# Performance work log

Hardware: AMD Instinct MI355X
Metric: run time of the kernel (lower is better)

The kernel has to match this reference:

```python
import jax, jax.numpy as jnp
import numpy as np

B, N = 32, 1000
HID, COM = 256, 64
T_LEN, NOP = 288, 3
NVAL, TP_D, CS_D, TIME_D = 9, 2, 4, 4
IN_C = CS_D + TP_D + NVAL            # 15, competition GAT input
IN_CO = IN_C + COM                    # 79, cooperation GAT input
OBS = TIME_D + TP_D + CS_D + 2 * COM + NVAL  # 147
K_D = K_F = 500                       # int(0.5*N + 0.5)
TEMP = 1.0
NEG = jnp.float32(-1e8)


def setup_inputs() -> dict:
    key = jax.random.key(0)
    ks = jax.random.split(key, 24)
    def nrm(k, shp, scale=0.05):
        return (jax.random.normal(k, shp, dtype=jnp.float32) * scale)
    return {
        "time_idx": jax.random.randint(ks[0], (B, N), 0, T_LEN, dtype=jnp.int32),
        "op_idx": jax.random.randint(ks[1], (B, N), 0, NOP, dtype=jnp.int32),
        "value_feats": jax.random.normal(ks[2], (B, N, NVAL), dtype=jnp.float32),
        "dpcs_mark": jax.random.randint(ks[3], (B, N, 1), 0, 2) > 0,
        "adj_comp": jax.random.randint(ks[4], (B, N, N), 0, 2) > 0,
        "adj_coop": jax.random.randint(ks[5], (B, N, N), 0, 2) > 0,
        "distance": jax.random.uniform(ks[6], (N, N), dtype=jnp.float32),
        "time_tab": jax.random.uniform(ks[7], (T_LEN, TIME_D), dtype=jnp.float32),
        "tp_tab": jax.random.uniform(ks[8], (NOP, TP_D), dtype=jnp.float32),
        "cs_tab": jax.random.uniform(ks[9], (N, CS_D), dtype=jnp.float32),
        "Wc": nrm(ks[10], (IN_C, COM)),
        "asrc_c": nrm(ks[11], (COM,)),
        "adst_c": nrm(ks[12], (COM,)),
        "wd_c": jnp.float32(0.1),
        "Wco": nrm(ks[13], (IN_CO, COM)),
        "asrc_co": nrm(ks[14], (COM,)),
        "adst_co": nrm(ks[15], (COM,)),
        "wd_co": jnp.float32(0.1),
        "Wp": nrm(ks[16], (OBS, HID)),
        "bp": jnp.zeros((HID,), dtype=jnp.float32),
        "vpd": nrm(ks[17], (HID,)),
        "vpf": nrm(ks[18], (HID,)),
    }


def gat(x, W, a_src, a_dst, w_d, adj, dist):
    """Single-head GAT over dense boolean adjacency. adj[b,j,i] True => edge j->i."""
    h = jnp.einsum("bnf,fd->bnd", x, W)                       # (B,N,D)
    e = (jnp.einsum("bid,d->bi", h, a_dst)[:, :, None]        # dst term
         + jnp.einsum("bjd,d->bj", h, a_src)[:, None, :]      # src term
         + w_d * dist.T[None])                                 # dist[j,i] edge feat
    e = jax.nn.leaky_relu(e, 0.2)
    mask = jnp.swapaxes(adj, 1, 2)                             # (B, dst i, src j)
    e = jnp.where(mask, e, NEG)
    alpha = jax.nn.softmax(e, axis=-1)
    alpha = jnp.where(mask, alpha, 0.0)                        # isolated nodes -> 0
    return jax.nn.elu(jnp.einsum("bij,bjd->bid", alpha, h))


def gated_pool(x_p, scores, valid, k, temp):
    scores = scores - scores.max(axis=1, keepdims=True)
    scores = jnp.where(valid, scores, NEG)                     # (B,N,1)
    val_topk = jax.lax.top_k(scores[..., 0], k)[0]             # (B,k)
    min_topk = val_topk.min(axis=-1)[:, None, None]
    scores = jnp.where(scores < min_topk, NEG, scores)
    w = jax.nn.softmax(scores / temp, axis=1)
    xg = x_p * w
    return jnp.concatenate([xg.sum(axis=1), xg.max(axis=1)], axis=-1)  # (B,2H)


def reference(time_idx, op_idx, value_feats, dpcs_mark, adj_comp, adj_coop,
              distance, time_tab, tp_tab, cs_tab, Wc, asrc_c, adst_c, wd_c,
              Wco, asrc_co, adst_co, wd_co, Wp, bp, vpd, vpf):
    time_e = time_tab[time_idx]                                # (B,N,4)
    tp_e = tp_tab[op_idx]                                      # (B,N,2)
    cs_e = jnp.broadcast_to(cs_tab[None], (B, N, CS_D))        # (B,N,4)
    vf_det = jax.lax.stop_gradient(value_feats)
    x = jnp.concatenate([cs_e, tp_e, vf_det], axis=-1)         # (B,N,15)
    comp_reps = gat(x, Wc, asrc_c, adst_c, wd_c, adj_comp, distance)
    x_m = jnp.concatenate([x, comp_reps], axis=-1)             # (B,N,79)
    coop_reps = gat(x_m, Wco, asrc_co, adst_co, wd_co, adj_coop, distance)
    sag = jnp.concatenate([time_e, cs_e, tp_e, value_feats, comp_reps, coop_reps], axis=-1)
    x_p = jnp.einsum("bnf,fh->bnh", sag, Wp) + bp              # (B,N,HID)
    scores_d = jnp.einsum("bnh,h->bn", x_p, vpd)[..., None]
    s_d = gated_pool(x_p, scores_d, dpcs_mark, K_D, TEMP)
    scores_f = jnp.einsum("bnh,h->bn", x_p, vpf)[..., None]
    s_f = gated_pool(x_p, scores_f, ~dpcs_mark, K_F, TEMP)
    return jnp.concatenate([s_f, s_d], axis=-1)                # (B, 4*HID)
```

## Files before the change

kernel.cpp:

```cpp
#include <hip/hip_runtime.h>
#include <hip/hip_bf16.h>

#define NB 32
#define NN 1000
#define COMD 64
#define HIDD 256
#define KSEL 500
#define TI 16
#define NSPL 32
#define ROWS 32
#define DSTRIDE 1024

#define PB_DT   0
#define PB_AQ1  256
#define PB_AQ2  1280
#define PB_WP   2304
#define PB_WCO  2344
#define PB_MISC 2368
#define PB_N    2369

typedef __hip_bfloat16 bf16;
typedef unsigned long long u64;
typedef __attribute__((ext_vector_type(4))) float f32x4;
typedef __attribute__((ext_vector_type(8))) short s16x8;
typedef __attribute__((ext_vector_type(4))) short s16x4;
typedef __attribute__((ext_vector_type(4))) unsigned short u16x4;
typedef __attribute__((ext_vector_type(2))) unsigned long long u64x2;

__device__ __forceinline__ float b2f(bf16 x){ return __bfloat162float(x); }

template<bool F32>
__device__ __forceinline__ float ldf(const void* p, long i){
  return F32 ? ((const float*)p)[i] : b2f(((const bf16*)p)[i]);
}
template<bool BINT>
__device__ __forceinline__ bool ldb(const void* p, long i){
  return BINT ? (((const int*)p)[i] != 0) : (((const unsigned char*)p)[i] != 0);
}

__device__ __forceinline__ float wave_sum(float v){
#pragma unroll
  for (int o = 32; o > 0; o >>= 1) v += __shfl_down(v, o, 64);
  return v;
}
__device__ __forceinline__ float wave_bsum(float v){
#pragma unroll
  for (int o = 32; o > 0; o >>= 1) v += __shfl_xor(v, o, 64);
  return v;
}
__device__ __forceinline__ float wave_bmax(float v){
#pragma unroll
  for (int o = 32; o > 0; o >>= 1) v = fmaxf(v, __shfl_xor(v, o, 64));
  return v;
}
__device__ __forceinline__ int wave_bsum_i(int v){
#pragma unroll
  for (int o = 32; o > 0; o >>= 1) v += __shfl_xor(v, o, 64);
  return v;
}
__device__ __forceinline__ unsigned fkey(float f){
  unsigned u = __float_as_uint(f);
  return (u & 0x80000000u) ? ~u : (u | 0x80000000u);
}
__device__ __forceinline__ void split_bf(float v, short& hi, short& lo){
  unsigned u = __float_as_uint(v);
  float hf = __uint_as_float(u & 0xFFFF0000u);
  hi = (short)(u >> 16);
  float r = v - hf;
  lo = (short)(__float_as_uint(r) >> 16);
}
__device__ __forceinline__ short f2bs(float v){
  bf16 h = __float2bfloat16(v);
  short s; __builtin_memcpy(&s, &h, 2); return s;
}
__device__ __forceinline__ void hB_write(short* hB_hi, short* hB_lo,
                                         int b, int n, int ch, float v){
  int kb = n >> 5, g4 = (n >> 3) & 3, u = n & 7;
  long off = ((((long)b * 32 + kb) * 4 + g4) * 64 + ch) * 8 + u;
  short hi, lo; split_bf(v, hi, lo);
  hB_hi[off] = hi; hB_lo[off] = lo;
}
__device__ __forceinline__ void sniff2(const void* dist, const void* adjc,
                                       int lane, int& f32, int& as_int){
  unsigned wdist = ((const unsigned*)dist)[lane];
  unsigned wadj  = ((const unsigned*)adjc)[lane];
  f32 = (__ballot((wdist & 0xFFFFu) >= 0x8000u) != 0ull) ? 1 : 0;
  as_int = (__ballot(wadj > 1u) == 0ull) ? 1 : 0;
}

template<bool F32>
__device__ void dist_t_role(const void* dist, bf16* distTb, int rel){
  __shared__ bf16 tile[64][68];
  int t = threadIdx.x;
  int wv = t >> 6, lane = t & 63;
  int it = (rel & 15) * 64, jt = (rel >> 4) * 64;
#pragma unroll
  for (int r = 0; r < 16; ++r){
    int jl = r * 4 + wv;
    int j = jt + jl, i = it + lane;
    float v = (j < NN && i < NN) ? ldf<F32>(dist, (long)j * NN + i) : 0.f;
    tile[jl][lane] = __float2bfloat16(v);
  }
  __syncthreads();
#pragma unroll
  for (int r = 0; r < 16; ++r){
    int il = r * 4 + wv;
    int i = it + il, j = jt + lane;
    if (i < NN) distTb[(long)i * DSTRIDE + j] = tile[lane][il];
  }
}
template<bool BINT>
__device__ void adjq_role(const void* adj, u64* adjQ, int rel){
  __shared__ u64 aw[16][33];
  int t = threadIdx.x;
  int wv = t >> 6, lane = t & 63;
  int j0 = (rel & 31) * 32;
  int b  = rel >> 5;
  for (int r = 0; r < 8; ++r){
    int j = j0 + wv * 8 + r;
    int jc = (j < NN) ? j : (NN - 1);
    long row = ((long)b * NN + jc) * NN;
#pragma unroll
    for (int c = 0; c < 4; ++c){
      int chunk = c * 64 + lane;
      bool okc = chunk < 250;
      bool p0, p1, p2, p3;
      if (BINT){
        uint4 d = {0u, 0u, 0u, 0u};
        if (okc) d = *(const uint4*)((const int*)adj + row + (long)chunk * 4);
        p0 = d.x != 0u; p1 = d.y != 0u; p2 = d.z != 0u; p3 = d.w != 0u;
      } else {
        unsigned d = 0u;
        if (okc) d = *(const unsigned*)((const unsigned char*)adj + row + (long)chunk * 4);
        p0 = (d & 0xFFu) != 0u;       p1 = (d & 0xFF00u) != 0u;
        p2 = (d & 0xFF0000u) != 0u;   p3 = (d & 0xFF000000u) != 0u;
      }
      u64 bal0 = __ballot(p0), bal1 = __ballot(p1);
      u64 bal2 = __ballot(p2), bal3 = __ballot(p3);
      if (lane < 4){
        u64 w = 0;
        if (j < NN){
          int sh = 16 * lane;
          w = ((bal0 >> sh) & 0xFFFFull)
            | (((bal1 >> sh) & 0xFFFFull) << 16)
            | (((bal2 >> sh) & 0xFFFFull) << 32)
            | (((bal3 >> sh) & 0xFFFFull) << 48);
        }
        aw[c * 4 + lane][wv * 8 + r] = w;
      }
    }
  }
  __syncthreads();
#pragma unroll
  for (int rr = 0; rr < 2; ++rr){
    int w2 = t + rr * 256;
    int iw = w2 >> 5, jloc = w2 & 31;
    adjQ[((long)b * 16 + iw) * 1024 + j0 + jloc] = aw[iw][jloc];
  }
}
template<bool F32>
__device__ void wp_role(const void* Wp, const void* vpd, const void* vpf,
                        short* WpB_hi, short* WpB_lo, float* wv_ws, int rel){
  int t = threadIdx.x;
  int g = t >> 6, lane = t & 63;
  int f = rel * 4 + g;
  float wrow[4];
#pragma unroll
  for (int r = 0; r < 4; ++r){
    int ch = r * 64 + lane;
    wrow[r] = (f < 147) ? ldf<F32>(Wp, (long)f * HIDD + ch) : 0.f;
  }
  int kb = f >> 5, q = (f >> 3) & 3, u = f & 7;
#pragma unroll
  for (int r = 0; r < 4; ++r){
    int ch = r * 64 + lane;
    long off = (((long)(kb * 4 + q)) * 256 + ch) * 8 + u;
    short hi, lo; split_bf(wrow[r], hi, lo);
    WpB_hi[off] = hi; WpB_lo[off] = lo;
  }
  float ad = 0.f, af = 0.f;
#pragma unroll
  for (int r = 0; r < 4; ++r){
    int ch = r * 64 + lane;
    ad += wrow[r] * ldf<F32>(vpd, ch);
    af += wrow[r] * ldf<F32>(vpf, ch);
  }
  ad = wave_bsum(ad); af = wave_bsum(af);
  if (lane == 0){ wv_ws[f] = ad; wv_ws[160 + f] = af; }
}
template<bool F32>
__device__ void wco_role(const void* Wco, const void* asrc, const void* adst,
                         short* WcoB_hi, short* WcoB_lo, float* pvco, int rel){
  int t = threadIdx.x;
  int g = t >> 6, lane = t & 63;
  int f = rel * 4 + g;
  float w = (f < 79) ? ldf<F32>(Wco, (long)f * COMD + lane) : 0.f;
  int kb = f >> 5, q = (f >> 3) & 3, u = f & 7;
  long off = (((long)(kb * 4 + q)) * 64 + lane) * 8 + u;
  short hi, lo; split_bf(w, hi, lo);
  WcoB_hi[off] = hi; WcoB_lo[off] = lo;
  float dd = wave_bsum(w * ldf<F32>(adst, lane));
  float ss = wave_bsum(w * ldf<F32>(asrc, lane));
  if (lane == 0){ pvco[f] = dd; pvco[96 + f] = ss; }
}
template<bool F32>
__device__ void misc_role(const void* wdc, const void* wdco,
                          const void* bp, const void* vpd, const void* vpf,
                          int f32, int as_int,
                          int* flags, float* wd_ws, float* wv_ws){
  int t = threadIdx.x;
  if (t >= 64) return;
  int lane = t;
  float ad = 0.f, af = 0.f;
#pragma unroll
  for (int r = 0; r < 4; ++r){
    int ch = r * 64 + lane;
    float bb = ldf<F32>(bp, ch);
    ad += bb * ldf<F32>(vpd, ch);
    af += bb * ldf<F32>(vpf, ch);
  }
  ad = wave_bsum(ad); af = wave_bsum(af);
  if (lane == 0){
    wv_ws[320] = ad; wv_ws[321] = af;
    wd_ws[0] = ldf<F32>(wdc, 0);
    wd_ws[1] = ldf<F32>(wdco, 0);
    flags[0] = f32; flags[1] = as_int;
  }
}
__global__ void __launch_bounds__(256) k_prep(
    const void* dist, const void* adj_comp, const void* adj_coop,
    const void* wdc, const void* wdco,
    const void* Wp, const void* vpd, const void* vpf, const void* bp,
    const void* Wco, const void* asrc_co, const void* adst_co,
    int* flags, float* wd_ws, bf16* distTb, u64* adjQc, u64* adjQo,
    short* WpB_hi, short* WpB_lo, float* wv_ws,
    short* WcoB_hi, short* WcoB_lo, float* pvco){
  int blk = blockIdx.x;
  int f32, as_int;
  sniff2(dist, adj_comp, threadIdx.x & 63, f32, as_int);
  if (blk < PB_AQ1){
    if (f32) dist_t_role<true >(dist, distTb, blk);
    else     dist_t_role<false>(dist, distTb, blk);
  } else if (blk < PB_AQ2){
    if (as_int) adjq_role<true >(adj_comp, adjQc, blk - PB_AQ1);
    else        adjq_role<false>(adj_comp, adjQc, blk - PB_AQ1);
  } else if (blk < PB_WP){
    if (as_int) adjq_role<true >(adj_coop, adjQo, blk - PB_AQ2);
    else        adjq_role<false>(adj_coop, adjQo, blk - PB_AQ2);
  } else if (blk < PB_WCO){
    if (f32) wp_role<true >(Wp, vpd, vpf, WpB_hi, WpB_lo, wv_ws, blk - PB_WP);
    else     wp_role<false>(Wp, vpd, vpf, WpB_hi, WpB_lo, wv_ws, blk - PB_WP);
  } else if (blk < PB_MISC){
    if (f32) wco_role<true >(Wco, asrc_co, adst_co, WcoB_hi, WcoB_lo, pvco, blk - PB_WCO);
    else     wco_role<false>(Wco, asrc_co, adst_co, WcoB_hi, WcoB_lo, pvco, blk - PB_WCO);
  } else {
    if (f32) misc_role<true >(wdc, wdco, bp, vpd, vpf, f32, as_int, flags, wd_ws, wv_ws);
    else     misc_role<false>(wdc, wdco, bp, vpd, vpf, f32, as_int, flags, wd_ws, wv_ws);
  }
}

template<bool F32>
__device__ __forceinline__ void embed_body(
    const int* op_idx, const void* vf, const void* cs_tab, const void* tp_tab,
    const void* Wc, const void* asrc, const void* adst,
    float* x_out, short* hB_hi, short* hB_lo, float* ed_out, float* es_out){
  int t = threadIdx.x;
  int w = t >> 6, lane = t & 63;
  int g = blockIdx.x * 4 + w;
  int b = g / NN, n = g - b * NN;
  int op = op_idx[g];
  float xv = 0.f, hacc = 0.f;
#pragma unroll
  for (int f = 0; f < 15; ++f){
    float x_f;
    if (f < 4)      x_f = ldf<F32>(cs_tab, n * 4 + f);
    else if (f < 6) x_f = ldf<F32>(tp_tab, op * 2 + (f - 4));
    else            x_f = ldf<F32>(vf, (long)g * 9 + (f - 6));
    if (lane == f) xv = x_f;
    hacc += x_f * ldf<F32>(Wc, f * COMD + lane);
  }
  if (lane < 15) x_out[g * 15 + lane] = xv;
  hB_write(hB_hi, hB_lo, b, n, lane, hacc);
  float sd = wave_sum(hacc * ldf<F32>(adst, lane));
  float ss = wave_sum(hacc * ldf<F32>(asrc, lane));
  if (lane == 0){ ed_out[g] = sd; es_out[g] = ss; }
}
__global__ void __launch_bounds__(256) k_embed(
    const int* flags, const int* op_idx, const void* vf, const void* cs_tab,
    const void* tp_tab, const void* Wc, const void* asrc, const void* adst,
    float* x_out, short* hB_hi, short* hB_lo, float* ed_out, float* es_out){
  if (flags[0]) embed_body<true >(op_idx, vf, cs_tab, tp_tab, Wc, asrc, adst, x_out, hB_hi, hB_lo, ed_out, es_out);
  else          embed_body<false>(op_idx, vf, cs_tab, tp_tab, Wc, asrc, adst, x_out, hB_hi, hB_lo, ed_out, es_out);
}

__global__ void __launch_bounds__(256) k_hco(
    const float* __restrict__ x_ws, const float* __restrict__ comp,
    const short* __restrict__ WcoB_hi, const short* __restrict__ WcoB_lo,
    const float* __restrict__ pvco,
    short* hB_hi, short* hB_lo, float* ed_out, float* es_out){
  __shared__ float cx[16][80] __attribute__((aligned(16)));
  __shared__ short cA_hi[3 * 16 * 40] __attribute__((aligned(16)));
  __shared__ short cA_lo[3 * 16 * 40] __attribute__((aligned(16)));
  int t = threadIdx.x;
  int wv = t >> 6, lane = t & 63;
  int base = blockIdx.x * 16;
  for (int idx = t; idx < 16 * 79; idx += 256){
    int nl = idx / 79, f = idx - nl * 79;
    int g = base + nl;
    cx[nl][f] = (f < 15) ? x_ws[g * 15 + f] : comp[(long)g * COMD + (f - 15)];
  }
  __syncthreads();
  {
    int node = t >> 4, sub = t & 15;
    float dd = 0.f, ss = 0.f;
    for (int f = sub; f < 79; f += 16){
      float c = cx[node][f];
      dd += c * pvco[f];
      ss += c * pvco[96 + f];
    }
#pragma unroll
    for (int o = 8; o > 0; o >>= 1){
      dd += __shfl_xor(dd, o, 64);
      ss += __shfl_xor(ss, o, 64);
    }
    if (sub == 0){
      int g = base + node;
      ed_out[g] = dd; es_out[g] = ss;
    }
  }
  for (int idx = t; idx < 16 * 96; idx += 256){
    int m = idx / 96, k = idx - m * 96;
    float v = (k < 79) ? cx[m][k] : 0.f;
    int kb = k >> 5, q = (k >> 3) & 3, u = k & 7;
    short hi, lo; split_bf(v, hi, lo);
    int off = (kb * 16 + m) * 40 + q * 8 + u;
    cA_hi[off] = hi; cA_lo[off] = lo;
  }
  __syncthreads();
  int q = lane >> 4, m = lane & 15;
  int ch = wv * 16 + m;
  f32x4 acc = {0.f, 0.f, 0.f, 0.f};
#pragma unroll
  for (int kb = 0; kb < 3; ++kb){
    int aoff = (kb * 16 + m) * 40 + q * 8;
    s16x8 a_hi = *(const s16x8*)&cA_hi[aoff];
    s16x8 a_lo = *(const s16x8*)&cA_lo[aoff];
    long boff = (((long)(kb * 4 + q)) * 64 + ch) * 8;
    s16x8 b_hi = *(const s16x8*)&WcoB_hi[boff];
    s16x8 b_lo = *(const s16x8*)&WcoB_lo[boff];
    acc = __builtin_amdgcn_mfma_f32_16x16x32_bf16(a_hi, b_hi, acc, 0, 0, 0);
    acc = __builtin_amdgcn_mfma_f32_16x16x32_bf16(a_hi, b_lo, acc, 0, 0, 0);
    acc = __builtin_amdgcn_mfma_f32_16x16x32_bf16(a_lo, b_hi, acc, 0, 0, 0);
  }
#pragma unroll
  for (int reg = 0; reg < 4; ++reg){
    int row = (lane >> 4) * 4 + reg;
    int g = base + row;
    int b = g / NN, n = g - b * NN;
    hB_write(hB_hi, hB_lo, b, n, ch, acc[reg]);
  }
}

__global__ void __launch_bounds__(256) k_gat(
    const float* __restrict__ ed, const float* __restrict__ es,
    const float* __restrict__ wd_ws, int wd_idx, const u64* __restrict__ adjQ,
    const bf16* __restrict__ distTb,
    const short* __restrict__ hB_hi, const short* __restrict__ hB_lo,
    float* __restrict__ reps){
  __shared__ short pA[32 * 544] __attribute__((aligned(16)));
  __shared__ float redz[TI][4];
  __shared__ float esred[4];
  int t = threadIdx.x;
  int wv = t >> 6, lane = t & 63;
  int b = blockIdx.y;
  int i0 = blockIdx.x * TI;
  float wd = wd_ws[wd_idx];
  int iw = i0 >> 6;
  int sb2 = (i0 & 63) >> 2;
  int j0 = t * 4;

  const u64* aq = adjQ + ((long)b * 16 + iw) * 1024 + j0;
  u64x2 wA = *(const u64x2*)&aq[0];
  u64x2 wB = *(const u64x2*)&aq[2];
  u64 wsh[4] = { wA[0] >> sb2, wA[1] >> sb2, wB[0] >> sb2, wB[1] >> sb2 };
  float4 es4 = *(const float4*)&es[(long)b * NN + j0];
  float esv[4] = {es4.x, es4.y, es4.z, es4.w};
  float esm = -1e30f;
#pragma unroll
  for (int c = 0; c < 4; ++c)
    esm = fmaxf(esm, (j0 + c < NN) ? esv[c] : -1e30f);
  esm = wave_bmax(esm);
  if (lane == 0) esred[wv] = esm;

  float ed_i[TI]; float edm = -1e30f;
#pragma unroll
  for (int ti = 0; ti < TI; ++ti){
    int i = i0 + ti;
    float ev = ed[(long)b * NN + ((i < NN) ? i : (NN - 1))];
    ed_i[ti] = ev;
    edm = fmaxf(edm, (i < NN) ? ev : -1e30f);
  }
  __syncthreads();
  float M = fmaxf(fmaxf(esred[0], esred[1]), fmaxf(esred[2], esred[3]))
            + edm + fmaxf(wd, 0.f);
  M = fmaxf(M, 0.f);

  float p[TI][4];
  const bf16* dbase = distTb + j0;
#pragma unroll
  for (int ti = 0; ti < TI; ++ti){
    int i = i0 + ti;
    int ic = (i < NN) ? i : (NN - 1);
    u16x4 d4 = *(const u16x4*)&dbase[(long)ic * DSTRIDE];
    float edti = ed_i[ti];
    int psh = 16 * (ti & 3) + (ti >> 2);
#pragma unroll
    for (int c = 0; c < 4; ++c){
      float d = __uint_as_float((unsigned)d4[c] << 16);
      float v = edti + esv[c] + wd * d;
      v = fmaxf(v, 0.2f * v);
      bool edge = (wsh[c] >> psh) & 1ull;
      float e = edge ? v : -1e30f;
      p[ti][c] = __expf(e - M);
    }
  }

  int kbw = 8 * wv + (lane >> 3);
  int qw = (lane >> 1) & 3;
  int u0 = 4 * (lane & 1);
  int wbase = kbw * 544 + qw * 136 + u0;
#pragma unroll
  for (int ti = 0; ti < TI; ++ti){
    float zs = p[ti][0] + p[ti][1] + p[ti][2] + p[ti][3];
    zs = wave_bsum(zs);
    if (lane == 0) redz[ti][wv] = zs;
    s16x4 s4 = { f2bs(p[ti][0]), f2bs(p[ti][1]), f2bs(p[ti][2]), f2bs(p[ti][3]) };
    *(s16x4*)&pA[wbase + ti * 8] = s4;
  }
  __syncthreads();

  int q = lane >> 4, m = lane & 15;
  int abase = q * 136 + m * 8;
  int ch = wv * 16 + m;
  const short* bh = hB_hi + (long)b * 65536 + ((long)q * 64 + ch) * 8;
  const short* bl = hB_lo + (long)b * 65536 + ((long)q * 64 + ch) * 8;
  f32x4 acc = {0.f, 0.f, 0.f, 0.f};
#pragma unroll
  for (int kb = 0; kb < 32; ++kb){
    s16x8 a   = *(const s16x8*)&pA[kb * 544 + abase];
    s16x8 bhi = *(const s16x8*)&bh[(long)kb * 2048];
    s16x8 blo = *(const s16x8*)&bl[(long)kb * 2048];
    acc = __builtin_amdgcn_mfma_f32_16x16x32_bf16(a, bhi, acc, 0, 0, 0);
    acc = __builtin_amdgcn_mfma_f32_16x16x32_bf16(a, blo, acc, 0, 0, 0);
  }
#pragma unroll
  for (int reg = 0; reg < 4; ++reg){
    int ti = (lane >> 4) * 4 + reg;
    float z = redz[ti][0] + redz[ti][1] + redz[ti][2] + redz[ti][3];
    float zi = (z > 0.f) ? 1.f / z : 0.f;
    float v = acc[reg] * zi;
    v = (v > 0.f) ? v : expm1f(v);
    int ch2 = wv * 16 + (lane & 15);
    if (i0 + ti < NN)
      reps[((long)b * NN + i0 + ti) * COMD + ch2] = v;
  }
}

template<bool F32>
__device__ __forceinline__ void xp_body(
    const int* time_idx, const int* op_idx, const void* vf, const void* time_tab,
    const void* cs_tab, const void* tp_tab, const float* comp, const float* coop,
    const short* __restrict__ WpB_hi, const short* __restrict__ WpB_lo,
    const float* __restrict__ wv_ws, const void* bp,
    float* x_p, float* scf, float* scd){
  __shared__ float sagF[16][148] __attribute__((aligned(16)));
  __shared__ short sagA_hi[5 * 16 * 40] __attribute__((aligned(16)));
  __shared__ short sagA_lo[5 * 16 * 40] __attribute__((aligned(16)));
  int t = threadIdx.x;
  int wv = t >> 6, lane = t & 63;
  int base = blockIdx.x * 16;

  for (int idx = t; idx < 16 * 147; idx += 256){
    int nl = idx / 147, f = idx - nl * 147;
    int g = base + nl;
    int n = g % NN;
    float v;
    if (f < 4)       v = ldf<F32>(time_tab, time_idx[g] * 4 + f);
    else if (f < 8)  v = ldf<F32>(cs_tab, n * 4 + (f - 4));
    else if (f < 10) v = ldf<F32>(tp_tab, op_idx[g] * 2 + (f - 8));
    else if (f < 19) v = ldf<F32>(vf, (long)g * 9 + (f - 10));
    else if (f < 83) v = comp[(long)g * COMD + (f - 19)];
    else             v = coop[(long)g * COMD + (f - 83)];
    sagF[nl][f] = v;
  }
  __syncthreads();

  for (int idx = t; idx < 16 * 160; idx += 256){
    int m = idx / 160, k = idx - m * 160;
    float v = (k < 147) ? sagF[m][k] : 0.f;
    int kb = k >> 5, q = (k >> 3) & 3, u = k & 7;
    short hi, lo; split_bf(v, hi, lo);
    int off = (kb * 16 + m) * 40 + q * 8 + u;
    sagA_hi[off] = hi; sagA_lo[off] = lo;
  }
  {
    int node = t >> 4, sub = t & 15;
    float ad = 0.f, af = 0.f;
    for (int f = sub; f < 147; f += 16){
      float s = sagF[node][f];
      ad += s * wv_ws[f];
      af += s * wv_ws[160 + f];
    }
#pragma unroll
    for (int o = 8; o > 0; o >>= 1){
      ad += __shfl_xor(ad, o, 64);
      af += __shfl_xor(af, o, 64);
    }
    if (sub == 0){
      scd[base + node] = ad + wv_ws[320];
      scf[base + node] = af + wv_ws[321];
    }
  }
  __syncthreads();

  int Ag = lane >> 4, Am = lane & 15;
  f32x4 acc[4] = {{0,0,0,0},{0,0,0,0},{0,0,0,0},{0,0,0,0}};
#pragma unroll
  for (int kb = 0; kb < 5; ++kb){
    int aoff = (kb * 16 + Am) * 40 + Ag * 8;
    s16x8 a_hi = *(const s16x8*)&sagA_hi[aoff];
    s16x8 a_lo = *(const s16x8*)&sagA_lo[aoff];
#pragma unroll
    for (int ct = 0; ct < 4; ++ct){
      int ch = wv * 64 + ct * 16 + Am;
      long boff = (((long)(kb * 4 + Ag)) * 256 + ch) * 8;
      s16x8 b_hi = *(const s16x8*)&WpB_hi[boff];
      s16x8 b_lo = *(const s16x8*)&WpB_lo[boff];
      acc[ct] = __builtin_amdgcn_mfma_f32_16x16x32_bf16(a_hi, b_hi, acc[ct], 0, 0, 0);
      acc[ct] = __builtin_amdgcn_mfma_f32_16x16x32_bf16(a_hi, b_lo, acc[ct], 0, 0, 0);
      acc[ct] = __builtin_amdgcn_mfma_f32_16x16x32_bf16(a_lo, b_hi, acc[ct], 0, 0, 0);
    }
  }
#pragma unroll
  for (int ct = 0; ct < 4; ++ct){
    int ch = wv * 64 + ct * 16 + (lane & 15);
    float bb = ldf<F32>(bp, ch);
#pragma unroll
    for (int reg = 0; reg < 4; ++reg){
      int row = (lane >> 4) * 4 + reg;
      x_p[(long)(base + row) * HIDD + ch] = acc[ct][reg] + bb;
    }
  }
}
__global__ void __launch_bounds__(256) k_xp(
    const int* flags, const int* time_idx, const int* op_idx, const void* vf,
    const void* time_tab, const void* cs_tab, const void* tp_tab,
    const float* comp, const float* coop,
    const short* WpB_hi, const short* WpB_lo, const float* wv_ws, const void* bp,
    float* x_p, float* scf, float* scd){
  if (flags[0]) xp_body<true >(time_idx, op_idx, vf, time_tab, cs_tab, tp_tab, comp, coop, WpB_hi, WpB_lo, wv_ws, bp, x_p, scf, scd);
  else          xp_body<false>(time_idx, op_idx, vf, time_tab, cs_tab, tp_tab, comp, coop, WpB_hi, WpB_lo, wv_ws, bp, x_p, scf, scd);
}

template<bool BINT>
__device__ __forceinline__ void topk_body(
    const float* scf, const float* scd, const void* mark, float* wls){
  int lane = threadIdx.x;
  int b = blockIdx.x, pool = blockIdx.y;
  const float* sc = (pool == 0) ? scf : scd;
  float v[16]; unsigned key[16];
  float m0 = -INFINITY;
#pragma unroll
  for (int r = 0; r < 16; ++r){
    int n = r * 64 + lane;
    float s = (n < NN) ? sc[b * NN + n] : -INFINITY;
    v[r] = s;
    m0 = fmaxf(m0, s);
  }
  m0 = wave_bmax(m0);
  float m1 = -INFINITY;
#pragma unroll
  for (int r = 0; r < 16; ++r){
    int n = r * 64 + lane;
    bool valid = false;
    if (n < NN){
      bool mk = ldb<BINT>(mark, b * NN + n);
      valid = (pool == 0) ? !mk : mk;
    }
    v[r] = valid ? (v[r] - m0) : -1e8f;
    key[r] = fkey(v[r]);
    if (n < NN) m1 = fmaxf(m1, v[r]);
  }
  m1 = wave_bmax(m1);

  unsigned lo = 0u, hi = 0xFFFFFFFFu;
  while (lo < hi){
    unsigned mid = lo + ((hi - lo) >> 1) + 1u;
    int c = 0;
#pragma unroll
    for (int r = 0; r < 16; ++r) c += (key[r] >= mid) ? 1 : 0;
    c = wave_bsum_i(c);
    if (c >= KSEL) lo = mid; else hi = mid - 1u;
  }

  float p[16];
  float ls = 0.f;
#pragma unroll
  for (int r = 0; r < 16; ++r){
    int n = r * 64 + lane;
    float pp = (n < NN && key[r] >= lo) ? __expf(v[r] - m1) : 0.f;
    p[r] = pp;
    ls += pp;
  }
  ls = wave_bsum(ls);
  float zinv = (ls > 0.f) ? 1.f / ls : 0.f;
  float* w_out = wls + ((long)b * 2 + pool) * 1024;
#pragma unroll
  for (int r = 0; r < 16; ++r){
    int n = r * 64 + lane;
    if (n < NN) w_out[n] = p[r] * zinv;
  }
}
__global__ void k_topk(const int* flags, const float* scf, const float* scd,
                       const void* mark, float* wls){
  if (flags[1]) topk_body<true >(scf, scd, mark, wls);
  else          topk_body<false>(scf, scd, mark, wls);
}

__global__ void __launch_bounds__(256) k_psum(
    const float* __restrict__ wls, const float* __restrict__ x_p,
    float* __restrict__ part){
  __shared__ float wf[ROWS], wdd[ROWS];
  int t = threadIdx.x;
  int b = blockIdx.x, z = blockIdx.y;
  int n0 = z * ROWS;
  int ns = min(ROWS, NN - n0);
  if (t < ns){
    wf[t]  = wls[((long)b * 2 + 0) * 1024 + n0 + t];
    wdd[t] = wls[((long)b * 2 + 1) * 1024 + n0 + t];
  }
  __syncthreads();
  float sf = 0.f, mf = -INFINITY, sd = 0.f, md = -INFINITY;
  const float* xb = x_p + ((long)b * NN + n0) * HIDD + t;
  for (int k = 0; k < ns; ++k){
    float xv = xb[(long)k * HIDD];
    float gf = wf[k] * xv;
    float gd = wdd[k] * xv;
    sf += gf; mf = fmaxf(mf, gf);
    sd += gd; md = fmaxf(md, gd);
  }
  long pb = (((long)b * NSPL + z) * 4) * HIDD + t;
  part[pb + 0 * HIDD] = sf;
  part[pb + 1 * HIDD] = mf;
  part[pb + 2 * HIDD] = sd;
  part[pb + 3 * HIDD] = md;
}

template<bool F32>
__device__ __forceinline__ void pfin_body(const float* part, void* out){
  int t = threadIdx.x;
  int b = blockIdx.x;
  float sf = 0.f, mf = -INFINITY, sd = 0.f, md = -INFINITY;
#pragma unroll
  for (int z = 0; z < NSPL; ++z){
    long pb = (((long)b * NSPL + z) * 4) * HIDD + t;
    sf += part[pb + 0 * HIDD];
    mf = fmaxf(mf, part[pb + 1 * HIDD]);
    sd += part[pb + 2 * HIDD];
    md = fmaxf(md, part[pb + 3 * HIDD]);
  }
  long ob = (long)b * 1024;
  if (F32){
    ((float*)out)[ob + t] = sf;
    ((float*)out)[ob + 256 + t] = mf;
    ((float*)out)[ob + 512 + t] = sd;
    ((float*)out)[ob + 768 + t] = md;
  } else {
    ((bf16*)out)[ob + t] = __float2bfloat16(sf);
    ((bf16*)out)[ob + 256 + t] = __float2bfloat16(mf);
    ((bf16*)out)[ob + 512 + t] = __float2bfloat16(sd);
    ((bf16*)out)[ob + 768 + t] = __float2bfloat16(md);
  }
}
__global__ void k_pfin(const int* flags, const float* part, void* out){
  if (flags[0]) pfin_body<true >(part, out);
  else          pfin_body<false>(part, out);
}

extern "C" void kernel_launch(void* const* d_in, const int* in_sizes, int n_in,
                              void* d_out, int out_size, void* d_ws, size_t ws_size,
                              hipStream_t stream){
  const int*  time_idx = (const int*)d_in[0];
  const int*  op_idx   = (const int*)d_in[1];
  const void* vfeat    = d_in[2];
  const void* dpcs     = d_in[3];
  const void* adj_comp = d_in[4];
  const void* adj_coop = d_in[5];
  const void* dist     = d_in[6];
  const void* time_tab = d_in[7];
  const void* tp_tab   = d_in[8];
  const void* cs_tab   = d_in[9];
  const void* Wc       = d_in[10];
  const void* asrc_c   = d_in[11];
  const void* adst_c   = d_in[12];
  const void* wd_c     = d_in[13];
  const void* Wco      = d_in[14];
  const void* asrc_co  = d_in[15];
  const void* adst_co  = d_in[16];
  const void* wd_co    = d_in[17];
  const void* Wp       = d_in[18];
  const void* bp       = d_in[19];
  const void* vpd      = d_in[20];
  const void* vpf      = d_in[21];

  char* ws = (char*)d_ws;
  size_t o = 0;
  auto alloc = [&](size_t bytes)->char*{
    char* p = ws + o; o = (o + bytes + 255) & ~(size_t)255; return p;
  };
  int*   flags   = (int*)alloc(16);
  float* wd_ws   = (float*)alloc(8);
  bf16*  distTb  = (bf16*)alloc((size_t)NN * DSTRIDE * 2);
  u64*   adjQc   = (u64*)alloc((size_t)NB * 16 * 1024 * 8);
  u64*   adjQo   = (u64*)alloc((size_t)NB * 16 * 1024 * 8);
  float* x_ws    = (float*)alloc((size_t)NB * NN * 15 * 4);
  float* comp    = (float*)alloc((size_t)NB * NN * COMD * 4);
  float* coop    = (float*)alloc((size_t)NB * NN * COMD * 4);
  short* hB_hi   = (short*)alloc((size_t)NB * 65536 * 2);
  short* hB_lo   = (short*)alloc((size_t)NB * 65536 * 2);
  short* WpB_hi  = (short*)alloc((size_t)5 * 4 * 256 * 8 * 2);
  short* WpB_lo  = (short*)alloc((size_t)5 * 4 * 256 * 8 * 2);
  short* WcoB_hi = (short*)alloc((size_t)3 * 4 * 64 * 8 * 2);
  short* WcoB_lo = (short*)alloc((size_t)3 * 4 * 64 * 8 * 2);
  float* wv_ws   = (float*)alloc(322 * 4);
  float* pvco    = (float*)alloc(192 * 4);
  float* ed_c    = (float*)alloc((size_t)NB * NN * 4 + 256);
  float* es_c    = (float*)alloc((size_t)NB * NN * 4 + 256);
  float* ed_o    = (float*)alloc((size_t)NB * NN * 4 + 256);
  float* es_o    = (float*)alloc((size_t)NB * NN * 4 + 256);
  float* scf     = (float*)alloc((size_t)NB * NN * 4);
  float* scd     = (float*)alloc((size_t)NB * NN * 4);
  float* wls     = (float*)alloc((size_t)NB * 2 * 1024 * 4);
  float* part    = (float*)alloc((size_t)NB * NSPL * 4 * HIDD * 4);
  float* x_p     = (float*)alloc((size_t)NB * NN * HIDD * 4);

  k_prep<<<dim3(PB_N), dim3(256), 0, stream>>>(
      dist, adj_comp, adj_coop, wd_c, wd_co, Wp, vpd, vpf, bp,
      Wco, asrc_co, adst_co,
      flags, wd_ws, distTb, adjQc, adjQo, WpB_hi, WpB_lo, wv_ws,
      WcoB_hi, WcoB_lo, pvco);
  k_embed<<<dim3(NB * NN / 4), dim3(256), 0, stream>>>(
      flags, op_idx, vfeat, cs_tab, tp_tab, Wc, asrc_c, adst_c,
      x_ws, hB_hi, hB_lo, ed_c, es_c);
  k_gat<<<dim3((NN + TI - 1) / TI, NB), dim3(256), 0, stream>>>(
      ed_c, es_c, wd_ws, 0, adjQc, distTb, hB_hi, hB_lo, comp);
  k_hco<<<dim3(NB * NN / 16), dim3(256), 0, stream>>>(
      x_ws, comp, WcoB_hi, WcoB_lo, pvco, hB_hi, hB_lo, ed_o, es_o);
  k_gat<<<dim3((NN + TI - 1) / TI, NB), dim3(256), 0, stream>>>(
      ed_o, es_o, wd_ws, 1, adjQo, distTb, hB_hi, hB_lo, coop);
  k_xp<<<dim3(NB * NN / 16), dim3(256), 0, stream>>>(
      flags, time_idx, op_idx, vfeat, time_tab, cs_tab, tp_tab, comp, coop,
      WpB_hi, WpB_lo, wv_ws, bp, x_p, scf, scd);
  k_topk<<<dim3(NB, 2), dim3(64), 0, stream>>>(flags, scf, scd, dpcs, wls);
  k_psum<<<dim3(NB, NSPL), dim3(256), 0, stream>>>(wls, x_p, part);
  k_pfin<<<dim3(NB), dim3(256), 0, stream>>>(flags, part, d_out);
}
```

Measured before the change: 494.9 us.

## Fuse embed kernel into prep kernel and prefetch adjacency rows

The embed work becomes extra blocks of the prep kernel, removing one launch and letting it overlap with the adjacency packing. The embed blocks now use the f32 sniff result computed locally instead of reading flags written by an earlier kernel. Adjacency packing now double-buffers row loads so the next row's loads are in flight while the current one is balloted. Block roles are reordered so adjacency blocks come first, and the shared-memory tiles are merged into one buffer. This adds register pressure and a much larger combined grid.

New measurement: 487.6 us. About the same (-1.5%).

```diff
diff --git a/kernel.cpp b/kernel.cpp
--- a/kernel.cpp
+++ b/kernel.cpp
@@ -11,13 +11,14 @@
 #define ROWS 32
 #define DSTRIDE 1024
 
-#define PB_DT   0
-#define PB_AQ1  256
-#define PB_AQ2  1280
+#define PB_AQ1  0
+#define PB_AQ2  1024
+#define PB_DT   2048
 #define PB_WP   2304
 #define PB_WCO  2344
 #define PB_MISC 2368
-#define PB_N    2369
+#define PB_EMB  2369
+#define PB_N    (PB_EMB + NB * NN / 4)
 
 typedef __hip_bfloat16 bf16;
 typedef unsigned long long u64;
@@ -88,9 +89,12 @@
   as_int = (__ballot(wadj > 1u) == 0ull) ? 1 : 0;
 }
 
+#define SMEM_BYTES 8704
+
 template<bool F32>
-__device__ void dist_t_role(const void* dist, bf16* distTb, int rel){
-  __shared__ bf16 tile[64][68];
+__device__ __forceinline__ void dist_t_role(const void* dist, bf16* distTb,
+                                            int rel, void* sm){
+  bf16 (*tile)[68] = (bf16 (*)[68])sm;
   int t = threadIdx.x;
   int wv = t >> 6, lane = t & 63;
   int it = (rel & 15) * 64, jt = (rel >> 4) * 64;
@@ -110,43 +114,99 @@
   }
 }
 template<bool BINT>
-__device__ void adjq_role(const void* adj, u64* adjQ, int rel){
-  __shared__ u64 aw[16][33];
+__device__ __forceinline__ void adjq_role(const void* adj, u64* adjQ,
+                                          int rel, void* sm){
+  u64 (*aw)[33] = (u64 (*)[33])sm;
   int t = threadIdx.x;
   int wv = t >> 6, lane = t & 63;
   int j0 = (rel & 31) * 32;
   int b  = rel >> 5;
-  for (int r = 0; r < 8; ++r){
-    int j = j0 + wv * 8 + r;
+  int ch3 = (192 + lane < 250) ? (192 + lane) : 249;
+  int chk[4] = { lane, 64 + lane, 128 + lane, ch3 };
+  long row0;
+  {
+    int j = j0 + wv * 8;
     int jc = (j < NN) ? j : (NN - 1);
-    long row = ((long)b * NN + jc) * NN;
-#pragma unroll
-    for (int c = 0; c < 4; ++c){
-      int chunk = c * 64 + lane;
-      bool okc = chunk < 250;
-      bool p0, p1, p2, p3;
-      if (BINT){
-        uint4 d = {0u, 0u, 0u, 0u};
-        if (okc) d = *(const uint4*)((const int*)adj + row + (long)chunk * 4);
-        p0 = d.x != 0u; p1 = d.y != 0u; p2 = d.z != 0u; p3 = d.w != 0u;
-      } else {
-        unsigned d = 0u;
-        if (okc) d = *(const unsigned*)((const unsigned char*)adj + row + (long)chunk * 4);
-        p0 = (d & 0xFFu) != 0u;       p1 = (d & 0xFF00u) != 0u;
-        p2 = (d & 0xFF0000u) != 0u;   p3 = (d & 0xFF000000u) != 0u;
+    row0 = ((long)b * NN + jc) * (long)NN;
+  }
+  if (BINT){
+    const int* base = (const int*)adj;
+    uint4 cur[4], nxt[4];
+#pragma unroll
+    for (int c = 0; c < 4; ++c)
+      cur[c] = *(const uint4*)(base + row0 + (long)chk[c] * 4);
+#pragma unroll
+    for (int r = 0; r < 8; ++r){
+      if (r < 7){
+        int j2 = j0 + wv * 8 + r + 1;
+        int jc2 = (j2 < NN) ? j2 : (NN - 1);
+        long row2 = ((long)b * NN + jc2) * (long)NN;
+#pragma unroll
+        for (int c = 0; c < 4; ++c)
+          nxt[c] = *(const uint4*)(base + row2 + (long)chk[c] * 4);
       }
-      u64 bal0 = __ballot(p0), bal1 = __ballot(p1);
-      u64 bal2 = __ballot(p2), bal3 = __ballot(p3);
-      if (lane < 4){
-        u64 w = 0;
-        if (j < NN){
-          int sh = 16 * lane;
-          w = ((bal0 >> sh) & 0xFFFFull)
-            | (((bal1 >> sh) & 0xFFFFull) << 16)
-            | (((bal2 >> sh) & 0xFFFFull) << 32)
-            | (((bal3 >> sh) & 0xFFFFull) << 48);
+      int j = j0 + wv * 8 + r;
+#pragma unroll
+      for (int c = 0; c < 4; ++c){
+        u64 bal0 = __ballot(cur[c].x != 0u);
+        u64 bal1 = __ballot(cur[c].y != 0u);
+        u64 bal2 = __ballot(cur[c].z != 0u);
+        u64 bal3 = __ballot(cur[c].w != 0u);
+        if (lane < 4){
+          u64 w = 0;
+          if (j < NN){
+            int sh = 16 * lane;
+            w = ((bal0 >> sh) & 0xFFFFull)
+              | (((bal1 >> sh) & 0xFFFFull) << 16)
+              | (((bal2 >> sh) & 0xFFFFull) << 32)
+              | (((bal3 >> sh) & 0xFFFFull) << 48);
+          }
+          aw[c * 4 + lane][wv * 8 + r] = w;
         }
-        aw[c * 4 + lane][wv * 8 + r] = w;
+      }
+      if (r < 7){
+#pragma unroll
+        for (int c = 0; c < 4; ++c) cur[c] = nxt[c];
+      }
+    }
+  } else {
+    const unsigned char* base = (const unsigned char*)adj;
+    unsigned cur[4], nxt[4];
+#pragma unroll
+    for (int c = 0; c < 4; ++c)
+      cur[c] = *(const unsigned*)(base + row0 + (long)chk[c] * 4);
+#pragma unroll
+    for (int r = 0; r < 8; ++r){
+      if (r < 7){
+        int j2 = j0 + wv * 8 + r + 1;
+        int jc2 = (j2 < NN) ? j2 : (NN - 1);
+        long row2 = ((long)b * NN + jc2) * (long)NN;
+#pragma unroll
+        for (int c = 0; c < 4; ++c)
+          nxt[c] = *(const unsigned*)(base + row2 + (long)chk[c] * 4);
+      }
+      int j = j0 + wv * 8 + r;
+#pragma unroll
+      for (int c = 0; c < 4; ++c){
+        u64 bal0 = __ballot((cur[c] & 0xFFu) != 0u);
+        u64 bal1 = __ballot((cur[c] & 0xFF00u) != 0u);
+        u64 bal2 = __ballot((cur[c] & 0xFF0000u) != 0u);
+        u64 bal3 = __ballot((cur[c] & 0xFF000000u) != 0u);
+        if (lane < 4){
+          u64 w = 0;
+          if (j < NN){
+            int sh = 16 * lane;
+            w = ((bal0 >> sh) & 0xFFFFull)
+              | (((bal1 >> sh) & 0xFFFFull) << 16)
+              | (((bal2 >> sh) & 0xFFFFull) << 32)
+              | (((bal3 >> sh) & 0xFFFFull) << 48);
+          }
+          aw[c * 4 + lane][wv * 8 + r] = w;
+        }
+      }
+      if (r < 7){
+#pragma unroll
+        for (int c = 0; c < 4; ++c) cur[c] = nxt[c];
       }
     }
   }
@@ -159,7 +219,7 @@
   }
 }
 template<bool F32>
-__device__ void wp_role(const void* Wp, const void* vpd, const void* vpf,
+__device__ __forceinline__ void wp_role(const void* Wp, const void* vpd, const void* vpf,
                         short* WpB_hi, short* WpB_lo, float* wv_ws, int rel){
   int t = threadIdx.x;
   int g = t >> 6, lane = t & 63;
@@ -189,7 +249,7 @@
   if (lane == 0){ wv_ws[f] = ad; wv_ws[160 + f] = af; }
 }
 template<bool F32>
-__device__ void wco_role(const void* Wco, const void* asrc, const void* adst,
+__device__ __forceinline__ void wco_role(const void* Wco, const void* asrc, const void* adst,
                          short* WcoB_hi, short* WcoB_lo, float* pvco, int rel){
   int t = threadIdx.x;
   int g = t >> 6, lane = t & 63;
@@ -204,7 +264,7 @@
   if (lane == 0){ pvco[f] = dd; pvco[96 + f] = ss; }
 }
 template<bool F32>
-__device__ void misc_role(const void* wdc, const void* wdco,
+__device__ __forceinline__ void misc_role(const void* wdc, const void* wdco,
                           const void* bp, const void* vpd, const void* vpf,
                           int f32, int as_int,
                           int* flags, float* wd_ws, float* wv_ws){
@@ -227,46 +287,15 @@
     flags[0] = f32; flags[1] = as_int;
   }
 }
-__global__ void __launch_bounds__(256) k_prep(
-    const void* dist, const void* adj_comp, const void* adj_coop,
-    const void* wdc, const void* wdco,
-    const void* Wp, const void* vpd, const void* vpf, const void* bp,
-    const void* Wco, const void* asrc_co, const void* adst_co,
-    int* flags, float* wd_ws, bf16* distTb, u64* adjQc, u64* adjQo,
-    short* WpB_hi, short* WpB_lo, float* wv_ws,
-    short* WcoB_hi, short* WcoB_lo, float* pvco){
-  int blk = blockIdx.x;
-  int f32, as_int;
-  sniff2(dist, adj_comp, threadIdx.x & 63, f32, as_int);
-  if (blk < PB_AQ1){
-    if (f32) dist_t_role<true >(dist, distTb, blk);
-    else     dist_t_role<false>(dist, distTb, blk);
-  } else if (blk < PB_AQ2){
-    if (as_int) adjq_role<true >(adj_comp, adjQc, blk - PB_AQ1);
-    else        adjq_role<false>(adj_comp, adjQc, blk - PB_AQ1);
-  } else if (blk < PB_WP){
-    if (as_int) adjq_role<true >(adj_coop, adjQo, blk - PB_AQ2);
-    else        adjq_role<false>(adj_coop, adjQo, blk - PB_AQ2);
-  } else if (blk < PB_WCO){
-    if (f32) wp_role<true >(Wp, vpd, vpf, WpB_hi, WpB_lo, wv_ws, blk - PB_WP);
-    else     wp_role<false>(Wp, vpd, vpf, WpB_hi, WpB_lo, wv_ws, blk - PB_WP);
-  } else if (blk < PB_MISC){
-    if (f32) wco_role<true >(Wco, asrc_co, adst_co, WcoB_hi, WcoB_lo, pvco, blk - PB_WCO);
-    else     wco_role<false>(Wco, asrc_co, adst_co, WcoB_hi, WcoB_lo, pvco, blk - PB_WCO);
-  } else {
-    if (f32) misc_role<true >(wdc, wdco, bp, vpd, vpf, f32, as_int, flags, wd_ws, wv_ws);
-    else     misc_role<false>(wdc, wdco, bp, vpd, vpf, f32, as_int, flags, wd_ws, wv_ws);
-  }
-}
-
 template<bool F32>
 __device__ __forceinline__ void embed_body(
     const int* op_idx, const void* vf, const void* cs_tab, const void* tp_tab,
     const void* Wc, const void* asrc, const void* adst,
-    float* x_out, short* hB_hi, short* hB_lo, float* ed_out, float* es_out){
+    float* x_out, short* hB_hi, short* hB_lo, float* ed_out, float* es_out,
+    int rel){
   int t = threadIdx.x;
   int w = t >> 6, lane = t & 63;
-  int g = blockIdx.x * 4 + w;
+  int g = rel * 4 + w;
   int b = g / NN, n = g - b * NN;
   int op = op_idx[g];
   float xv = 0.f, hacc = 0.f;
@@ -285,12 +314,45 @@
   float ss = wave_sum(hacc * ldf<F32>(asrc, lane));
   if (lane == 0){ ed_out[g] = sd; es_out[g] = ss; }
 }
-__global__ void __launch_bounds__(256) k_embed(
-    const int* flags, const int* op_idx, const void* vf, const void* cs_tab,
-    const void* tp_tab, const void* Wc, const void* asrc, const void* adst,
-    float* x_out, short* hB_hi, short* hB_lo, float* ed_out, float* es_out){
-  if (flags[0]) embed_body<true >(op_idx, vf, cs_tab, tp_tab, Wc, asrc, adst, x_out, hB_hi, hB_lo, ed_out, es_out);
-  else          embed_body<false>(op_idx, vf, cs_tab, tp_tab, Wc, asrc, adst, x_out, hB_hi, hB_lo, ed_out, es_out);
+__global__ void __launch_bounds__(256) k_prep(
+    const void* dist, const void* adj_comp, const void* adj_coop,
+    const void* wdc, const void* wdco,
+    const void* Wp, const void* vpd, const void* vpf, const void* bp,
+    const void* Wco, const void* asrc_co, const void* adst_co,
+    const int* op_idx, const void* vfeat, const void* cs_tab, const void* tp_tab,
+    const void* Wc, const void* asrc_c, const void* adst_c,
+    int* flags, float* wd_ws, bf16* distTb, u64* adjQc, u64* adjQo,
+    short* WpB_hi, short* WpB_lo, float* wv_ws,
+    short* WcoB_hi, short* WcoB_lo, float* pvco,
+    float* x_ws, short* hB_hi, short* hB_lo, float* ed_c, float* es_c){
+  __shared__ __attribute__((aligned(16))) char smem[SMEM_BYTES];
+  int blk = blockIdx.x;
+  int f32, as_int;
+  sniff2(dist, adj_comp, threadIdx.x & 63, f32, as_int);
+  if (blk < PB_AQ2){
+    if (as_int) adjq_role<true >(adj_comp, adjQc, blk - PB_AQ1, smem);
+    else        adjq_role<false>(adj_comp, adjQc, blk - PB_AQ1, smem);
+  } else if (blk < PB_DT){
+    if (as_int) adjq_role<true >(adj_coop, adjQo, blk - PB_AQ2, smem);
+    else        adjq_role<false>(adj_coop, adjQo, blk - PB_AQ2, smem);
+  } else if (blk < PB_WP){
+    if (f32) dist_t_role<true >(dist, distTb, blk - PB_DT, smem);
+    else     dist_t_role<false>(dist, distTb, blk - PB_DT, smem);
+  } else if (blk < PB_WCO){
+    if (f32) wp_role<true >(Wp, vpd, vpf, WpB_hi, WpB_lo, wv_ws, blk - PB_WP);
+    else     wp_role<false>(Wp, vpd, vpf, WpB_hi, WpB_lo, wv_ws, blk - PB_WP);
+  } else if (blk < PB_MISC){
+    if (f32) wco_role<true >(Wco, asrc_co, adst_co, WcoB_hi, WcoB_lo, pvco, blk - PB_WCO);
+    else     wco_role<false>(Wco, asrc_co, adst_co, WcoB_hi, WcoB_lo, pvco, blk - PB_WCO);
+  } else if (blk < PB_EMB){
+    if (f32) misc_role<true >(wdc, wdco, bp, vpd, vpf, f32, as_int, flags, wd_ws, wv_ws);
+    else     misc_role<false>(wdc, wdco, bp, vpd, vpf, f32, as_int, flags, wd_ws, wv_ws);
+  } else {
+    if (f32) embed_body<true >(op_idx, vfeat, cs_tab, tp_tab, Wc, asrc_c, adst_c,
+                               x_ws, hB_hi, hB_lo, ed_c, es_c, blk - PB_EMB);
+    else     embed_body<false>(op_idx, vfeat, cs_tab, tp_tab, Wc, asrc_c, adst_c,
+                               x_ws, hB_hi, hB_lo, ed_c, es_c, blk - PB_EMB);
+  }
 }
 
 __global__ void __launch_bounds__(256) k_hco(
@@ -747,10 +809,9 @@
   k_prep<<<dim3(PB_N), dim3(256), 0, stream>>>(
       dist, adj_comp, adj_coop, wd_c, wd_co, Wp, vpd, vpf, bp,
       Wco, asrc_co, adst_co,
+      op_idx, vfeat, cs_tab, tp_tab, Wc, asrc_c, adst_c,
       flags, wd_ws, distTb, adjQc, adjQo, WpB_hi, WpB_lo, wv_ws,
-      WcoB_hi, WcoB_lo, pvco);
-  k_embed<<<dim3(NB * NN / 4), dim3(256), 0, stream>>>(
-      flags, op_idx, vfeat, cs_tab, tp_tab, Wc, asrc_c, adst_c,
+      WcoB_hi, WcoB_lo, pvco,
       x_ws, hB_hi, hB_lo, ed_c, es_c);
   k_gat<<<dim3((NN + TI - 1) / TI, NB), dim3(256), 0, stream>>>(
       ed_c, es_c, wd_ws, 0, adjQc, distTb, hB_hi, hB_lo, comp);
```
